# Performance work log

Measured on AMD Instinct MI355X. Metric: run time of the kernel, lower is better.

Reference implementation:

```python
import jax, jax.numpy as jnp
import numpy as np

B, S, D, H = 2, 2048, 1024, 16
HEAD_DIM = D // H  # 64


def setup_inputs() -> dict:
    key = jax.random.key(0)
    ks = jax.random.split(key, 7)
    x = jax.random.normal(ks[0], (B, S, D), dtype=jnp.float32)
    W_q = jax.random.normal(ks[1], (D, D), dtype=jnp.float32) * 0.02
    W_k = jax.random.normal(ks[2], (D, D), dtype=jnp.float32) * 0.02
    W_v = jax.random.normal(ks[3], (D, D), dtype=jnp.float32) * 0.02
    W_o = jax.random.normal(ks[4], (D, D), dtype=jnp.float32) * 0.02 / np.sqrt(2 * 12)
    b_o = jnp.zeros((D,), dtype=jnp.float32)
    # Ragged prefix attention_mask: per-row valid lengths in [S/2, S];
    # row 0 forced to full length so max_valid_len == S statically (jit-safe).
    lengths = jax.random.randint(ks[5], (B,), S // 2, S + 1)
    lengths = lengths.at[0].set(S)
    attention_mask = (jnp.arange(S)[None, :] < lengths[:, None]).astype(jnp.float32)
    return {"x": x, "attention_mask": attention_mask, "W_q": W_q, "W_k": W_k,
            "W_v": W_v, "W_o": W_o, "b_o": b_o}


def reference(x, attention_mask, W_q, W_k, W_v, W_o, b_o):
    b, s, d = x.shape
    h, hd = H, HEAD_DIM
    # QKV projections (no bias, qkv_bias=False)
    q = (x @ W_q.T).reshape(b, s, h, hd).transpose(0, 2, 1, 3)  # [b,h,s,hd]
    # Masking keys/values at invalid (padded) positions; for prefix masks this
    # is exactly the module's per-batch packing loop (max_valid_len == s).
    m = attention_mask[:, None, :, None]  # [b,1,s,1]
    k = ((x @ W_k.T).reshape(b, s, h, hd).transpose(0, 2, 1, 3)) * m
    v = ((x @ W_v.T).reshape(b, s, h, hd).transpose(0, 2, 1, 3)) * m
    # Naive causal attention, same op order as the torch module:
    # mask with -inf first, then scale by 1/sqrt(head_dim), then softmax.
    causal = jnp.triu(jnp.ones((s, s), dtype=bool), 1)  # True above diagonal
    scores = jnp.einsum('bhqd,bhkd->bhqk', q, k)
    scores = jnp.where(causal[None, None], -jnp.inf, scores)
    att = jax.nn.softmax(scores / jnp.sqrt(jnp.float32(hd)), axis=-1)
    ctx = jnp.einsum('bhqk,bhkd->bhqd', att, v)  # [b,h,s,hd]
    ctx = ctx.transpose(0, 2, 1, 3).reshape(b, s, d)
    # Output projection (dropout is inference no-op)
    return ctx @ W_o.T + b_o
```

## Files before the change

kernel.cpp:

```cpp
#include <hip/hip_runtime.h>

#define B_  2
#define S_  2048
#define D_  1024
#define H_  16
#define HD_ 64
#define N3_ 3072
#define M_  4096

typedef _Float16 f16;
typedef _Float16 f16x2 __attribute__((ext_vector_type(2)));
typedef _Float16 f16x4 __attribute__((ext_vector_type(4)));
typedef _Float16 f16x8 __attribute__((ext_vector_type(8)));
typedef float    f32x4 __attribute__((ext_vector_type(4)));

__device__ __forceinline__ void async16(const f16* g, f16* l) {
  __builtin_amdgcn_global_load_lds(
      (const __attribute__((address_space(1))) unsigned int*)g,
      (__attribute__((address_space(3))) unsigned int*)l, 16, 0, 0);
}

__device__ __forceinline__ f16x2 pkrtz(float a, float b) {
  return __builtin_bit_cast(f16x2, __builtin_amdgcn_cvt_pkrtz(a, b));
}

__global__ __launch_bounds__(256)
void cvt_f32_f16(const float* __restrict__ src, f16* __restrict__ dst,
                 int n4, float scale) {
  int i = blockIdx.x * 256 + threadIdx.x;
  if (i >= n4) return;
  float4 v = ((const float4*)src)[i];
  f16x4 o = { (f16)(v.x * scale), (f16)(v.y * scale),
              (f16)(v.z * scale), (f16)(v.w * scale) };
  ((f16x4*)dst)[i] = o;
}

__global__ __launch_bounds__(256)
void cvt_weights(const float* __restrict__ Wq, const float* __restrict__ Wk,
                 const float* __restrict__ Wv, const float* __restrict__ Wo,
                 f16* __restrict__ dst, float qscale) {
  const int m = blockIdx.y;
  const float* src = (m == 0) ? Wq : (m == 1) ? Wk : (m == 2) ? Wv : Wo;
  const float scale = (m == 0) ? qscale : 1.0f;
  int i = blockIdx.x * 256 + threadIdx.x;
  float4 v = ((const float4*)src)[i];
  f16x4 o = { (f16)(v.x * scale), (f16)(v.y * scale),
              (f16)(v.z * scale), (f16)(v.w * scale) };
  ((f16x4*)(dst + (size_t)m * D_ * D_))[i] = o;
}

template<int QKV>
__global__ __launch_bounds__(256)
void gemm_nt(const f16* __restrict__ A, const f16* __restrict__ Bw,
             f16* __restrict__ Cq, float* __restrict__ Cf,
             f16* __restrict__ vtout,
             const float* __restrict__ mask, const float* __restrict__ bias,
             int Ndim, int Kdim) {
  __shared__ f16 As[2][128 * 64];
  __shared__ f16 Bs[2][128 * 64];

  const int tid  = threadIdx.x;
  const int lane = tid & 63;
  const int w    = tid >> 6;
  const int lcol = lane & 15;
  const int quad = lane >> 4;
  const int lx   = lcol & 7;
  const int wave_m = w >> 1, wave_n = w & 1;

  const int m0 = blockIdx.y * 128;
  const int n0 = blockIdx.x * 128;

  const int rr  = lane >> 3;
  const int gch = (lane & 7) ^ rr;

  const f16* gA[4];
  const f16* gB[4];
  int soff[4];
#pragma unroll
  for (int i = 0; i < 4; i++) {
    int seg = i * 4 + w;
    int row = seg * 8 + rr;
    gA[i] = A  + (size_t)(m0 + row) * Kdim + gch * 8;
    gB[i] = Bw + (size_t)(n0 + row) * Kdim + gch * 8;
    soff[i] = seg * 512;
  }

  auto stage = [&](int k0, int buf) {
#pragma unroll
    for (int i = 0; i < 4; i++) async16(gA[i] + k0, As[buf] + soff[i]);
#pragma unroll
    for (int i = 0; i < 4; i++) async16(gB[i] + k0, Bs[buf] + soff[i]);
  };

  int offA[4], offB[4];
#pragma unroll
  for (int i = 0; i < 4; i++) {
    offA[i] = (wave_m * 64 + i * 16 + lcol) * 64;
    offB[i] = (wave_n * 64 + i * 16 + lcol) * 64;
  }

  const f32x4 zero = {0.f, 0.f, 0.f, 0.f};
  f32x4 acc[4][4];
#pragma unroll
  for (int i = 0; i < 4; i++)
#pragma unroll
    for (int j = 0; j < 4; j++) acc[i][j] = zero;

  const int niter = Kdim >> 6;
  stage(0, 0);
  for (int it = 0; it < niter; it++) {
    __syncthreads();
    if (it + 1 < niter) stage((it + 1) << 6, (it + 1) & 1);

    const f16* Ab = As[it & 1];
    const f16* Bb = Bs[it & 1];
#pragma unroll
    for (int ks = 0; ks < 2; ks++) {
      const int co = ((quad + 4 * ks) ^ lx) * 8;
      f16x8 af[4], bf[4];
#pragma unroll
      for (int i = 0; i < 4; i++) af[i] = *(const f16x8*)(Ab + offA[i] + co);
#pragma unroll
      for (int i = 0; i < 4; i++) bf[i] = *(const f16x8*)(Bb + offB[i] + co);
#pragma unroll
      for (int mi = 0; mi < 4; mi++)
#pragma unroll
        for (int ni = 0; ni < 4; ni++)
          acc[mi][ni] = __builtin_amdgcn_mfma_f32_16x16x32_f16(
              af[mi], bf[ni], acc[mi][ni], 0, 0, 0);
    }
  }

  if (QKV && n0 >= 2 * D_) {
#pragma unroll
    for (int mi = 0; mi < 4; mi++) {
      const int mgb = m0 + wave_m * 64 + mi * 16 + quad * 4;
      const int b = mgb >> 11, s = mgb & (S_ - 1);
      const float mk0 = mask[mgb], mk1 = mask[mgb + 1];
      const float mk2 = mask[mgb + 2], mk3 = mask[mgb + 3];
#pragma unroll
      for (int ni = 0; ni < 4; ni++) {
        const int vcol = n0 - 2 * D_ + wave_n * 64 + ni * 16 + lcol;
        f16x4 v = { (f16)(acc[mi][ni][0] * mk0), (f16)(acc[mi][ni][1] * mk1),
                    (f16)(acc[mi][ni][2] * mk2), (f16)(acc[mi][ni][3] * mk3) };
        *(f16x4*)(vtout +
                  ((size_t)(b * 16 + (vcol >> 6)) * 64 + (vcol & 63)) * S_ + s) = v;
      }
    }
  } else {
    const bool kmask = QKV && (n0 >= D_);
#pragma unroll
    for (int mi = 0; mi < 4; mi++) {
#pragma unroll
      for (int r = 0; r < 4; r++) {
        int mg = m0 + wave_m * 64 + mi * 16 + quad * 4 + r;
        float mk = kmask ? mask[mg] : 1.0f;
#pragma unroll
        for (int ni = 0; ni < 4; ni++) {
          int ng = n0 + wave_n * 64 + ni * 16 + lcol;
          float v = acc[mi][ni][r] * mk;
          if (QKV) Cq[(size_t)mg * Ndim + ng] = (f16)v;
          else     Cf[(size_t)mg * Ndim + ng] = v + bias[ng];
        }
      }
    }
  }
}

__global__ __launch_bounds__(256)
void flash_attn5(const f16* __restrict__ qkv, const f16* __restrict__ vt,
                 f16* __restrict__ ctx) {
  __shared__ f16 Ks[2][64 * 64];
  __shared__ f16 Vs[2][64 * 64];

  const int tid  = threadIdx.x;
  const int lane = tid & 63;
  const int w    = tid >> 6;
  const int lcol = lane & 15;
  const int quad = lane >> 4;
  const int lx   = lcol & 7;

  const int id   = blockIdx.x;
  const int bh   = (id & 7) + 8 * ((id >> 3) & 3);
  const int pair = id >> 5;
  const int b    = bh >> 4, h = bh & 15;
  const int qtA  = 31 - pair;
  const int qtB  = pair;

  const int rsub = lane >> 3;
  const int gch  = (lane & 7) ^ rsub;
  const int ko0  = (w * 8) * 64;
  const int ko1  = (32 + w * 8) * 64;
  const int krow0 = w * 8 + rsub;
  const int krow1 = 32 + w * 8 + rsub;
  const f16* Kg = qkv + (size_t)b * S_ * N3_ + D_ + h * HD_;
  const f16* Vg = vt + (size_t)bh * HD_ * S_;

  auto stage = [&](int kt, int buf) {
    const int kbase = kt * 64;
    async16(Kg + (size_t)(kbase + krow0) * N3_ + gch * 8, Ks[buf] + ko0);
    async16(Kg + (size_t)(kbase + krow1) * N3_ + gch * 8, Ks[buf] + ko1);
    async16(Vg + (size_t)krow0 * S_ + kbase + gch * 8, Vs[buf] + ko0);
    async16(Vg + (size_t)krow1 * S_ + kbase + gch * 8, Vs[buf] + ko1);
  };

  const f32x4 zero = {0.f, 0.f, 0.f, 0.f};

  const int qrowA = qtA * 64 + w * 16 + lcol;
  const int qrowB = qtB * 64 + w * 16 + lcol;
  const f16* QpA = qkv + (size_t)(b * S_ + qrowA) * N3_ + h * HD_;
  const f16* QpB = qkv + (size_t)(b * S_ + qrowB) * N3_ + h * HD_;
  const f16x8 qbA0 = *(const f16x8*)(QpA + quad * 8);
  const f16x8 qbA1 = *(const f16x8*)(QpA + 32 + quad * 8);
  const f16x8 qbB0 = *(const f16x8*)(QpB + quad * 8);
  const f16x8 qbB1 = *(const f16x8*)(QpB + 32 + quad * 8);

  f32x4 oA[4], oB[4];
  float lpA = 0.f, lpB = 0.f;
#pragma unroll
  for (int i = 0; i < 4; i++) { oA[i] = zero; oB[i] = zero; }

  auto mask_diag = [&](f32x4* sc) {
#pragma unroll
    for (int ct = 0; ct < 4; ct++) {
      int koff = ct * 16 + quad * 4;
      int qoff = w * 16 + lcol;
#pragma unroll
      for (int r = 0; r < 4; r++)
        if (koff + r > qoff) sc[ct][r] = -1e30f;
    }
  };
  auto softmax_tiles = [&](f32x4* sc, f16x4* pf, float& lp) {
#pragma unroll
    for (int ct = 0; ct < 4; ct++) {
      float e0 = exp2f(sc[ct][0]);
      float e1 = exp2f(sc[ct][1]);
      float e2 = exp2f(sc[ct][2]);
      float e3 = exp2f(sc[ct][3]);
      lp += (e0 + e1) + (e2 + e3);
      f16x2 lo = pkrtz(e0, e1);
      f16x2 hi = pkrtz(e2, e3);
      f16x4 p = { lo[0], lo[1], hi[0], hi[1] };
      pf[ct] = p;
    }
  };

  stage(0, 0);
  for (int kt = 0; kt <= qtA; kt++) {
    __syncthreads();
    if (kt + 1 <= qtA) stage(kt + 1, (kt + 1) & 1);

    const f16* Kb = Ks[kt & 1];
    const f16* Vb = Vs[kt & 1];
    const bool doB = (kt <= qtB);

    f16x8 kf0[4], kf1[4];
    f32x4 scA[4], scB[4];
#pragma unroll
    for (int ct = 0; ct < 4; ct++) {
      const f16* kr = Kb + (ct * 16 + lcol) * 64;
      kf0[ct] = *(const f16x8*)(kr + ((quad    ) ^ lx) * 8);
      kf1[ct] = *(const f16x8*)(kr + ((quad + 4) ^ lx) * 8);
      f32x4 z = zero;
      z = __builtin_amdgcn_mfma_f32_16x16x32_f16(kf0[ct], qbA0, z, 0, 0, 0);
      z = __builtin_amdgcn_mfma_f32_16x16x32_f16(kf1[ct], qbA1, z, 0, 0, 0);
      scA[ct] = z;
    }
    if (doB) {
#pragma unroll
      for (int ct = 0; ct < 4; ct++) {
        f32x4 z = zero;
        z = __builtin_amdgcn_mfma_f32_16x16x32_f16(kf0[ct], qbB0, z, 0, 0, 0);
        z = __builtin_amdgcn_mfma_f32_16x16x32_f16(kf1[ct], qbB1, z, 0, 0, 0);
        scB[ct] = z;
      }
    }

    if (kt == qtA) mask_diag(scA);
    if (doB && kt == qtB) mask_diag(scB);

    f16x4 pfA[4], pfB[4];
    softmax_tiles(scA, pfA, lpA);
    if (doB) softmax_tiles(scB, pfB, lpB);

#pragma unroll
    for (int ht = 0; ht < 4; ht++) {
      const f16* vr = Vb + (ht * 16 + lcol) * 64 + (quad & 1) * 4;
      f16x4 vf[4];
#pragma unroll
      for (int ct = 0; ct < 4; ct++)
        vf[ct] = *(const f16x4*)(vr + (((2 * ct + (quad >> 1)) ^ lx) * 8));
#pragma unroll
      for (int ct = 0; ct < 4; ct++)
        oA[ht] = __builtin_amdgcn_mfma_f32_16x16x16f16(vf[ct], pfA[ct], oA[ht], 0, 0, 0);
      if (doB) {
#pragma unroll
        for (int ct = 0; ct < 4; ct++)
          oB[ht] = __builtin_amdgcn_mfma_f32_16x16x16f16(vf[ct], pfB[ct], oB[ht], 0, 0, 0);
      }
    }
  }

  lpA += __shfl_xor(lpA, 16);
  lpA += __shfl_xor(lpA, 32);
  lpB += __shfl_xor(lpB, 16);
  lpB += __shfl_xor(lpB, 32);
  const float invA = 1.f / lpA;
  const float invB = 1.f / lpB;
  f16* cpA = ctx + (size_t)(b * S_ + qrowA) * D_ + h * HD_ + quad * 4;
  f16* cpB = ctx + (size_t)(b * S_ + qrowB) * D_ + h * HD_ + quad * 4;
#pragma unroll
  for (int ht = 0; ht < 4; ht++) {
    f16x4 ovA = { (f16)(oA[ht][0] * invA), (f16)(oA[ht][1] * invA),
                  (f16)(oA[ht][2] * invA), (f16)(oA[ht][3] * invA) };
    *(f16x4*)(cpA + ht * 16) = ovA;
    f16x4 ovB = { (f16)(oB[ht][0] * invB), (f16)(oB[ht][1] * invB),
                  (f16)(oB[ht][2] * invB), (f16)(oB[ht][3] * invB) };
    *(f16x4*)(cpB + ht * 16) = ovB;
  }
}

extern "C" void kernel_launch(void* const* d_in, const int* in_sizes, int n_in,
                              void* d_out, int out_size, void* d_ws, size_t ws_size,
                              hipStream_t stream) {
  (void)in_sizes; (void)n_in; (void)out_size; (void)ws_size;
  const float* x  = (const float*)d_in[0];
  const float* am = (const float*)d_in[1];
  const float* Wq = (const float*)d_in[2];
  const float* Wk = (const float*)d_in[3];
  const float* Wv = (const float*)d_in[4];
  const float* Wo = (const float*)d_in[5];
  const float* bo = (const float*)d_in[6];
  float* out = (float*)d_out;

  f16* ws   = (f16*)d_ws;
  f16* wqkv = ws;
  f16* wo16 = wqkv + (size_t)3 * D_ * D_;
  f16* xb   = wo16 + (size_t)D_ * D_;
  f16* qkvb = xb + (size_t)M_ * D_;
  f16* vtb  = qkvb + (size_t)M_ * N3_;
  f16* ctxb = vtb + (size_t)M_ * D_;

  const float qscale = 0.125f * 1.4426950408889634f;

  cvt_f32_f16<<<dim3(M_ * D_ / 1024), 256, 0, stream>>>(x, xb, M_ * D_ / 4, 1.0f);
  cvt_weights<<<dim3(D_ * D_ / 1024, 4), 256, 0, stream>>>(Wq, Wk, Wv, Wo, wqkv, qscale);

  gemm_nt<1><<<dim3(N3_ / 128, M_ / 128), 256, 0, stream>>>(
      xb, wqkv, qkvb, nullptr, vtb, am, nullptr, N3_, D_);
  flash_attn5<<<dim3(512), 256, 0, stream>>>(qkvb, vtb, ctxb);
  gemm_nt<0><<<dim3(D_ / 128, M_ / 128), 256, 0, stream>>>(
      ctxb, wo16, nullptr, out, nullptr, nullptr, bo, D_, D_);
}
```

Baseline: 196.3 us.

## Merge conversion kernels, split GEMMs, single-buffer attention, MFMA row sums

Folds the x and weight fp32-to-fp16 conversions into one launch. Splits the templated GEMM into a QKV kernel and an output-projection kernel; the projection uses 64-row tiles, which doubles the grid to 512 blocks for better occupancy. In attention, the double-buffered K/V staging becomes a single buffer with load-then-sync each iteration, which frees LDS but removes load/compute overlap. The softmax row sum is now computed with an MFMA against a ones vector instead of scalar adds and shuffles.

```diff
diff --git a/kernel.cpp b/kernel.cpp
--- a/kernel.cpp
+++ b/kernel.cpp
@@ -25,37 +25,37 @@
 }
 
 __global__ __launch_bounds__(256)
-void cvt_f32_f16(const float* __restrict__ src, f16* __restrict__ dst,
-                 int n4, float scale) {
-  int i = blockIdx.x * 256 + threadIdx.x;
-  if (i >= n4) return;
-  float4 v = ((const float4*)src)[i];
+void cvt_all(const float* __restrict__ x,
+             const float* __restrict__ Wq, const float* __restrict__ Wk,
+             const float* __restrict__ Wv, const float* __restrict__ Wo,
+             f16* __restrict__ xb, f16* __restrict__ wdst, float qscale) {
+  const int i = blockIdx.x * 256 + threadIdx.x;
+  const int XN4 = M_ * D_ / 4;
+  const int WN4 = D_ * D_ / 4;
+  const float* src;
+  f16* dst;
+  float scale = 1.0f;
+  int j;
+  if (i < XN4) {
+    src = x; dst = xb; j = i;
+  } else {
+    int k = i - XN4;
+    int m = k >> 18;
+    j = k & (WN4 - 1);
+    src = (m == 0) ? Wq : (m == 1) ? Wk : (m == 2) ? Wv : Wo;
+    if (m == 0) scale = qscale;
+    dst = wdst + (size_t)m * D_ * D_;
+  }
+  float4 v = ((const float4*)src)[j];
   f16x4 o = { (f16)(v.x * scale), (f16)(v.y * scale),
               (f16)(v.z * scale), (f16)(v.w * scale) };
-  ((f16x4*)dst)[i] = o;
+  ((f16x4*)dst)[j] = o;
 }
 
 __global__ __launch_bounds__(256)
-void cvt_weights(const float* __restrict__ Wq, const float* __restrict__ Wk,
-                 const float* __restrict__ Wv, const float* __restrict__ Wo,
-                 f16* __restrict__ dst, float qscale) {
-  const int m = blockIdx.y;
-  const float* src = (m == 0) ? Wq : (m == 1) ? Wk : (m == 2) ? Wv : Wo;
-  const float scale = (m == 0) ? qscale : 1.0f;
-  int i = blockIdx.x * 256 + threadIdx.x;
-  float4 v = ((const float4*)src)[i];
-  f16x4 o = { (f16)(v.x * scale), (f16)(v.y * scale),
-              (f16)(v.z * scale), (f16)(v.w * scale) };
-  ((f16x4*)(dst + (size_t)m * D_ * D_))[i] = o;
-}
-
-template<int QKV>
-__global__ __launch_bounds__(256)
-void gemm_nt(const f16* __restrict__ A, const f16* __restrict__ Bw,
-             f16* __restrict__ Cq, float* __restrict__ Cf,
-             f16* __restrict__ vtout,
-             const float* __restrict__ mask, const float* __restrict__ bias,
-             int Ndim, int Kdim) {
+void gemm_qkv(const f16* __restrict__ A, const f16* __restrict__ Bw,
+              f16* __restrict__ Cq, f16* __restrict__ vtout,
+              const float* __restrict__ mask) {
   __shared__ f16 As[2][128 * 64];
   __shared__ f16 Bs[2][128 * 64];
 
@@ -80,8 +80,8 @@
   for (int i = 0; i < 4; i++) {
     int seg = i * 4 + w;
     int row = seg * 8 + rr;
-    gA[i] = A  + (size_t)(m0 + row) * Kdim + gch * 8;
-    gB[i] = Bw + (size_t)(n0 + row) * Kdim + gch * 8;
+    gA[i] = A  + (size_t)(m0 + row) * D_ + gch * 8;
+    gB[i] = Bw + (size_t)(n0 + row) * D_ + gch * 8;
     soff[i] = seg * 512;
   }
 
@@ -106,7 +106,7 @@
 #pragma unroll
     for (int j = 0; j < 4; j++) acc[i][j] = zero;
 
-  const int niter = Kdim >> 6;
+  const int niter = D_ >> 6;
   stage(0, 0);
   for (int it = 0; it < niter; it++) {
     __syncthreads();
@@ -131,7 +131,7 @@
     }
   }
 
-  if (QKV && n0 >= 2 * D_) {
+  if (n0 >= 2 * D_) {
 #pragma unroll
     for (int mi = 0; mi < 4; mi++) {
       const int mgb = m0 + wave_m * 64 + mi * 16 + quad * 4;
@@ -148,7 +148,7 @@
       }
     }
   } else {
-    const bool kmask = QKV && (n0 >= D_);
+    const bool kmask = (n0 >= D_);
 #pragma unroll
     for (int mi = 0; mi < 4; mi++) {
 #pragma unroll
@@ -158,9 +158,7 @@
 #pragma unroll
         for (int ni = 0; ni < 4; ni++) {
           int ng = n0 + wave_n * 64 + ni * 16 + lcol;
-          float v = acc[mi][ni][r] * mk;
-          if (QKV) Cq[(size_t)mg * Ndim + ng] = (f16)v;
-          else     Cf[(size_t)mg * Ndim + ng] = v + bias[ng];
+          Cq[(size_t)mg * N3_ + ng] = (f16)(acc[mi][ni][r] * mk);
         }
       }
     }
@@ -168,10 +166,10 @@
 }
 
 __global__ __launch_bounds__(256)
-void flash_attn5(const f16* __restrict__ qkv, const f16* __restrict__ vt,
-                 f16* __restrict__ ctx) {
-  __shared__ f16 Ks[2][64 * 64];
-  __shared__ f16 Vs[2][64 * 64];
+void gemm_proj(const f16* __restrict__ A, const f16* __restrict__ Bw,
+               float* __restrict__ Cf, const float* __restrict__ bias) {
+  __shared__ f16 As[2][64 * 64];
+  __shared__ f16 Bs[2][128 * 64];
 
   const int tid  = threadIdx.x;
   const int lane = tid & 63;
@@ -179,6 +177,101 @@
   const int lcol = lane & 15;
   const int quad = lane >> 4;
   const int lx   = lcol & 7;
+  const int wave_m = w >> 1, wave_n = w & 1;
+
+  const int m0 = blockIdx.y * 64;
+  const int n0 = blockIdx.x * 128;
+
+  const int rr  = lane >> 3;
+  const int gch = (lane & 7) ^ rr;
+
+  const f16* gA[2];
+  const f16* gB[4];
+  int sA[2], sB[4];
+#pragma unroll
+  for (int i = 0; i < 2; i++) {
+    int seg = 2 * w + i;
+    gA[i] = A + (size_t)(m0 + seg * 8 + rr) * D_ + gch * 8;
+    sA[i] = seg * 512;
+  }
+#pragma unroll
+  for (int i = 0; i < 4; i++) {
+    int seg = i * 4 + w;
+    gB[i] = Bw + (size_t)(n0 + seg * 8 + rr) * D_ + gch * 8;
+    sB[i] = seg * 512;
+  }
+
+  auto stage = [&](int k0, int buf) {
+#pragma unroll
+    for (int i = 0; i < 2; i++) async16(gA[i] + k0, As[buf] + sA[i]);
+#pragma unroll
+    for (int i = 0; i < 4; i++) async16(gB[i] + k0, Bs[buf] + sB[i]);
+  };
+
+  int offA[2], offB[4];
+#pragma unroll
+  for (int i = 0; i < 2; i++) offA[i] = (wave_m * 32 + i * 16 + lcol) * 64;
+#pragma unroll
+  for (int i = 0; i < 4; i++) offB[i] = (wave_n * 64 + i * 16 + lcol) * 64;
+
+  const f32x4 zero = {0.f, 0.f, 0.f, 0.f};
+  f32x4 acc[2][4];
+#pragma unroll
+  for (int i = 0; i < 2; i++)
+#pragma unroll
+    for (int j = 0; j < 4; j++) acc[i][j] = zero;
+
+  const int niter = D_ >> 6;
+  stage(0, 0);
+  for (int it = 0; it < niter; it++) {
+    __syncthreads();
+    if (it + 1 < niter) stage((it + 1) << 6, (it + 1) & 1);
+
+    const f16* Ab = As[it & 1];
+    const f16* Bb = Bs[it & 1];
+#pragma unroll
+    for (int ks = 0; ks < 2; ks++) {
+      const int co = ((quad + 4 * ks) ^ lx) * 8;
+      f16x8 af[2], bf[4];
+#pragma unroll
+      for (int i = 0; i < 2; i++) af[i] = *(const f16x8*)(Ab + offA[i] + co);
+#pragma unroll
+      for (int i = 0; i < 4; i++) bf[i] = *(const f16x8*)(Bb + offB[i] + co);
+#pragma unroll
+      for (int mi = 0; mi < 2; mi++)
+#pragma unroll
+        for (int ni = 0; ni < 4; ni++)
+          acc[mi][ni] = __builtin_amdgcn_mfma_f32_16x16x32_f16(
+              af[mi], bf[ni], acc[mi][ni], 0, 0, 0);
+    }
+  }
+
+#pragma unroll
+  for (int mi = 0; mi < 2; mi++) {
+#pragma unroll
+    for (int r = 0; r < 4; r++) {
+      int mg = m0 + wave_m * 32 + mi * 16 + quad * 4 + r;
+#pragma unroll
+      for (int ni = 0; ni < 4; ni++) {
+        int ng = n0 + wave_n * 64 + ni * 16 + lcol;
+        Cf[(size_t)mg * D_ + ng] = acc[mi][ni][r] + bias[ng];
+      }
+    }
+  }
+}
+
+__global__ __launch_bounds__(256)
+void flash_attn6(const f16* __restrict__ qkv, const f16* __restrict__ vt,
+                 f16* __restrict__ ctx) {
+  __shared__ f16 Ks[64 * 64];
+  __shared__ f16 Vs[64 * 64];
+
+  const int tid  = threadIdx.x;
+  const int lane = tid & 63;
+  const int w    = tid >> 6;
+  const int lcol = lane & 15;
+  const int quad = lane >> 4;
+  const int lx   = lcol & 7;
 
   const int id   = blockIdx.x;
   const int bh   = (id & 7) + 8 * ((id >> 3) & 3);
@@ -189,20 +282,14 @@
 
   const int rsub = lane >> 3;
   const int gch  = (lane & 7) ^ rsub;
-  const int ko0  = (w * 8) * 64;
-  const int ko1  = (32 + w * 8) * 64;
   const int krow0 = w * 8 + rsub;
   const int krow1 = 32 + w * 8 + rsub;
   const f16* Kg = qkv + (size_t)b * S_ * N3_ + D_ + h * HD_;
   const f16* Vg = vt + (size_t)bh * HD_ * S_;
-
-  auto stage = [&](int kt, int buf) {
-    const int kbase = kt * 64;
-    async16(Kg + (size_t)(kbase + krow0) * N3_ + gch * 8, Ks[buf] + ko0);
-    async16(Kg + (size_t)(kbase + krow1) * N3_ + gch * 8, Ks[buf] + ko1);
-    async16(Vg + (size_t)krow0 * S_ + kbase + gch * 8, Vs[buf] + ko0);
-    async16(Vg + (size_t)krow1 * S_ + kbase + gch * 8, Vs[buf] + ko1);
-  };
+  f16* ldsK0 = Ks + (w * 8) * 64;
+  f16* ldsK1 = Ks + (32 + w * 8) * 64;
+  f16* ldsV0 = Vs + (w * 8) * 64;
+  f16* ldsV1 = Vs + (32 + w * 8) * 64;
 
   const f32x4 zero = {0.f, 0.f, 0.f, 0.f};
 
@@ -216,9 +303,12 @@
   const f16x8 qbB1 = *(const f16x8*)(QpB + 32 + quad * 8);
 
   f32x4 oA[4], oB[4];
-  float lpA = 0.f, lpB = 0.f;
+  f32x4 sumA = zero, sumB = zero;
 #pragma unroll
   for (int i = 0; i < 4; i++) { oA[i] = zero; oB[i] = zero; }
+
+  const f16 one_h = (f16)(lcol == 0 ? 1.0f : 0.0f);
+  const f16x4 af_ones = { one_h, one_h, one_h, one_h };
 
   auto mask_diag = [&](f32x4* sc) {
 #pragma unroll
@@ -230,35 +320,33 @@
         if (koff + r > qoff) sc[ct][r] = -1e30f;
     }
   };
-  auto softmax_tiles = [&](f32x4* sc, f16x4* pf, float& lp) {
+  auto softmax_tiles = [&](f32x4* sc, f16x4* pf, f32x4& sum) {
 #pragma unroll
     for (int ct = 0; ct < 4; ct++) {
-      float e0 = exp2f(sc[ct][0]);
-      float e1 = exp2f(sc[ct][1]);
-      float e2 = exp2f(sc[ct][2]);
-      float e3 = exp2f(sc[ct][3]);
-      lp += (e0 + e1) + (e2 + e3);
-      f16x2 lo = pkrtz(e0, e1);
-      f16x2 hi = pkrtz(e2, e3);
+      f16x2 lo = pkrtz(exp2f(sc[ct][0]), exp2f(sc[ct][1]));
+      f16x2 hi = pkrtz(exp2f(sc[ct][2]), exp2f(sc[ct][3]));
       f16x4 p = { lo[0], lo[1], hi[0], hi[1] };
       pf[ct] = p;
+      sum = __builtin_amdgcn_mfma_f32_16x16x16f16(af_ones, p, sum, 0, 0, 0);
     }
   };
 
-  stage(0, 0);
   for (int kt = 0; kt <= qtA; kt++) {
+    const int kbase = kt * 64;
     __syncthreads();
-    if (kt + 1 <= qtA) stage(kt + 1, (kt + 1) & 1);
-
-    const f16* Kb = Ks[kt & 1];
-    const f16* Vb = Vs[kt & 1];
+    async16(Kg + (size_t)(kbase + krow0) * N3_ + gch * 8, ldsK0);
+    async16(Kg + (size_t)(kbase + krow1) * N3_ + gch * 8, ldsK1);
+    async16(Vg + (size_t)krow0 * S_ + kbase + gch * 8, ldsV0);
+    async16(Vg + (size_t)krow1 * S_ + kbase + gch * 8, ldsV1);
+    __syncthreads();
+
     const bool doB = (kt <= qtB);
 
     f16x8 kf0[4], kf1[4];
     f32x4 scA[4], scB[4];
 #pragma unroll
     for (int ct = 0; ct < 4; ct++) {
-      const f16* kr = Kb + (ct * 16 + lcol) * 64;
+      const f16* kr = Ks + (ct * 16 + lcol) * 64;
       kf0[ct] = *(const f16x8*)(kr + ((quad    ) ^ lx) * 8);
       kf1[ct] = *(const f16x8*)(kr + ((quad + 4) ^ lx) * 8);
       f32x4 z = zero;
@@ -280,12 +368,12 @@
     if (doB && kt == qtB) mask_diag(scB);
 
     f16x4 pfA[4], pfB[4];
-    softmax_tiles(scA, pfA, lpA);
-    if (doB) softmax_tiles(scB, pfB, lpB);
+    softmax_tiles(scA, pfA, sumA);
+    if (doB) softmax_tiles(scB, pfB, sumB);
 
 #pragma unroll
     for (int ht = 0; ht < 4; ht++) {
-      const f16* vr = Vb + (ht * 16 + lcol) * 64 + (quad & 1) * 4;
+      const f16* vr = Vs + (ht * 16 + lcol) * 64 + (quad & 1) * 4;
       f16x4 vf[4];
 #pragma unroll
       for (int ct = 0; ct < 4; ct++)
@@ -301,10 +389,8 @@
     }
   }
 
-  lpA += __shfl_xor(lpA, 16);
-  lpA += __shfl_xor(lpA, 32);
-  lpB += __shfl_xor(lpB, 16);
-  lpB += __shfl_xor(lpB, 32);
+  const float lpA = __shfl(sumA[0], lcol);
+  const float lpB = __shfl(sumB[0], lcol);
   const float invA = 1.f / lpA;
   const float invB = 1.f / lpB;
   f16* cpA = ctx + (size_t)(b * S_ + qrowA) * D_ + h * HD_ + quad * 4;
@@ -343,12 +429,12 @@
 
   const float qscale = 0.125f * 1.4426950408889634f;
 
-  cvt_f32_f16<<<dim3(M_ * D_ / 1024), 256, 0, stream>>>(x, xb, M_ * D_ / 4, 1.0f);
-  cvt_weights<<<dim3(D_ * D_ / 1024, 4), 256, 0, stream>>>(Wq, Wk, Wv, Wo, wqkv, qscale);
-
-  gemm_nt<1><<<dim3(N3_ / 128, M_ / 128), 256, 0, stream>>>(
-      xb, wqkv, qkvb, nullptr, vtb, am, nullptr, N3_, D_);
-  flash_attn5<<<dim3(512), 256, 0, stream>>>(qkvb, vtb, ctxb);
-  gemm_nt<0><<<dim3(D_ / 128, M_ / 128), 256, 0, stream>>>(
-      ctxb, wo16, nullptr, out, nullptr, nullptr, bo, D_, D_);
-}
+  cvt_all<<<dim3((M_ * D_ + 4 * D_ * D_) / 1024), 256, 0, stream>>>(
+      x, Wq, Wk, Wv, Wo, xb, wqkv, qscale);
+
+  gemm_qkv<<<dim3(N3_ / 128, M_ / 128), 256, 0, stream>>>(
+      xb, wqkv, qkvb, vtb, am);
+  flash_attn6<<<dim3(512), 256, 0, stream>>>(qkvb, vtb, ctxb);
+  gemm_proj<<<dim3(D_ / 128, M_ / 64), 256, 0, stream>>>(
+      ctxb, wo16, out, bo);
+}
```

Measured after the change: 200.0 us. No clear change (+1.9%).
